# Optimization experiments

Hardware: AMD Instinct MI355X
Metric: run time of the kernel (lower is better)

The kernel has to match this reference:

```python
import jax, jax.numpy as jnp
import numpy as np

H = 512   # n_hidden
V = 32000 # n_words
T1 = 128  # encoder length
T2 = 64   # decoder length
B = 32    # batch


def _gru_cell(x, h, W_ih, W_hh, b_ih, b_hh):
    # PyTorch GRUCell math. x: [B, in], h: [B, H]
    gi = x @ W_ih.T + b_ih            # [B, 3H]
    gh = h @ W_hh.T + b_hh            # [B, 3H]
    i_r, i_z, i_n = jnp.split(gi, 3, axis=-1)
    h_r, h_z, h_n = jnp.split(gh, 3, axis=-1)
    r = jax.nn.sigmoid(i_r + h_r)
    z = jax.nn.sigmoid(i_z + h_z)
    n = jnp.tanh(i_n + r * h_n)
    return (1.0 - z) * n + z * h


def setup_inputs() -> dict:
    key = jax.random.key(0)
    ks = jax.random.split(key, 18)
    s = 0.05
    f32 = jnp.float32
    return {
        "decoder_inputs": jax.random.randint(ks[0], (T2, B), 0, V),
        "state": jax.random.normal(ks[1], (2, B, H), f32),
        "encoder_outputs": jax.random.normal(ks[2], (T1, B, H), f32),
        "emb": jax.random.normal(ks[3], (V, H), f32) * s,
        "wa_W": jax.random.normal(ks[4], (H, 2 * H), f32) * s,
        "wa_b": jax.random.normal(ks[5], (H,), f32) * s,
        "va_W": jax.random.normal(ks[6], (1, H), f32) * s,
        "W_ih0": jax.random.normal(ks[7], (3 * H, 2 * H), f32) * s,
        "W_hh0": jax.random.normal(ks[8], (3 * H, H), f32) * s,
        "b_ih0": jax.random.normal(ks[9], (3 * H,), f32) * s,
        "b_hh0": jax.random.normal(ks[10], (3 * H,), f32) * s,
        "W_ih1": jax.random.normal(ks[11], (3 * H, H), f32) * s,
        "W_hh1": jax.random.normal(ks[12], (3 * H, H), f32) * s,
        "b_ih1": jax.random.normal(ks[13], (3 * H,), f32) * s,
        "b_hh1": jax.random.normal(ks[14], (3 * H,), f32) * s,
        "out_W": jax.random.normal(ks[15], (V, H), f32) * s,
        "out_b": jax.random.normal(ks[16], (V,), f32) * s,
    }


def reference(decoder_inputs, state, encoder_outputs, emb, wa_W, wa_b, va_W,
              W_ih0, W_hh0, b_ih0, b_hh0, W_ih1, W_hh1, b_ih1, b_hh1,
              out_W, out_b):
    x = emb[decoder_inputs]                               # [T2, B, H]
    # wa(concat([xt_rep, enc])) == xt @ Wx.T + enc @ We.T + b  (split the weight)
    Wx = wa_W[:, :H]                                      # [H, H]
    We = wa_W[:, H:]                                      # [H, H]
    enc_proj = jnp.einsum('tbh,oh->tbo', encoder_outputs, We) + wa_b  # [T1,B,H]
    va = va_W[0]                                          # [H]

    def step(h, xt):  # h: [2,B,H], xt: [B,H]
        u = jnp.tanh(xt @ Wx.T + enc_proj)                # [T1, B, H]
        e = jnp.einsum('tbh,h->tb', u, va)                # [T1, B]
        score = jax.nn.softmax(e, axis=0)                 # softmax over T1
        att_v = jnp.einsum('tbh,tb->bh', encoder_outputs, score)  # [B, H]
        gin = jnp.concatenate([xt, att_v], axis=-1)       # [B, 2H]
        h0 = _gru_cell(gin, h[0], W_ih0, W_hh0, b_ih0, b_hh0)
        h1 = _gru_cell(h0, h[1], W_ih1, W_hh1, b_ih1, b_hh1)
        return jnp.stack([h0, h1]), (h1, score)

    h_final, (ys, scores) = jax.lax.scan(step, state, x)  # ys: [T2, B, H]
    y = jnp.einsum('tbh,vh->tbv', ys, out_W) + out_b      # [T2, B, V]
    last_score = scores[-1][:, :, None]                   # [T1, B, 1] (torch returns last-step score)
    return y, h_final, last_score
```

## Files before the change

kernel.cpp:

```cpp
#include <hip/hip_runtime.h>
#include <hip/hip_bf16.h>
#include <hip/hip_cooperative_groups.h>
#include <stdint.h>

namespace cg = cooperative_groups;

#define HH   512
#define VV   32000
#define T1N  128
#define T2N  64
#define BB   32

typedef __attribute__((ext_vector_type(8))) short short8;
typedef __attribute__((ext_vector_type(4))) float f32x4;

__device__ __forceinline__ ushort f2b(float f) {
  unsigned u = __float_as_uint(f);
  unsigned r = (u + 0x7fffu + ((u >> 16) & 1u)) >> 16;
  return (ushort)r;
}
__device__ __forceinline__ float blo(unsigned u){ return __uint_as_float(u << 16); }
__device__ __forceinline__ float bhi(unsigned u){ return __uint_as_float(u & 0xffff0000u); }

__device__ __forceinline__ float fast_tanh(float x) {
  float ax = fabsf(x);
  float e  = __expf(-2.f * ax);
  float t  = (1.f - e) / (1.f + e);
  return x < 0.f ? -t : t;
}
__device__ __forceinline__ float fsig(float x) { return 1.f / (1.f + __expf(-x)); }

__global__ __launch_bounds__(256) void k_cvt(const float* __restrict__ s, ushort* __restrict__ d, int n) {
  int i = (blockIdx.x * 256 + threadIdx.x) * 4;
  if (i < n) {
    float4 v = *(const float4*)(s + i);
    ushort4 o = { f2b(v.x), f2b(v.y), f2b(v.z), f2b(v.w) };
    *(ushort4*)(d + i) = o;
  }
}

__global__ __launch_bounds__(256) void k_cvt_wa(const float* __restrict__ wa,
                                                ushort* __restrict__ Wx, ushort* __restrict__ We) {
  int i = (blockIdx.x * 256 + threadIdx.x) * 4;
  int half = (i >= HH * HH);
  int j = i & (HH * HH - 1);
  int o = j >> 9, c = j & 511;
  const float* s = wa + (size_t)o * 1024 + c + (half ? 512 : 0);
  float4 v = *(const float4*)s;
  ushort4 ov = { f2b(v.x), f2b(v.y), f2b(v.z), f2b(v.w) };
  *(ushort4*)((half ? We : Wx) + j) = ov;
}

__global__ __launch_bounds__(256) void k_embed(const int* __restrict__ toks, const float* __restrict__ emb,
                                               ushort* __restrict__ ginB) {
  int i = (blockIdx.x * 256 + threadIdx.x) * 4;
  int row = i >> 9, c = i & 511;
  int tok = toks[row];
  float4 v = *(const float4*)(emb + (size_t)tok * HH + c);
  ushort4 ov = { f2b(v.x), f2b(v.y), f2b(v.z), f2b(v.w) };
  *(ushort4*)(ginB + (size_t)row * 1024 + c) = ov;
}

__global__ __launch_bounds__(256) void k_gemm(const ushort* __restrict__ A, int lda,
                                              const ushort* __restrict__ B,
                                              const float* __restrict__ bias,
                                              float* __restrict__ C, int ldc, int K) {
  __shared__ ushort sA[128 * 32];
  __shared__ ushort sB[128 * 32];
  const int tid  = threadIdx.x;
  const int bm   = blockIdx.y * 128;
  const int bn   = blockIdx.x * 128;
  const int lane = tid & 63;
  const int wave = tid >> 6;
  const int wm   = (wave >> 1) * 64;
  const int wn   = (wave & 1) * 64;
  const int m16  = lane & 15;
  const int quad = lane >> 4;

  f32x4 acc[4][4] = {};

  for (int k0 = 0; k0 < K; k0 += 32) {
#pragma unroll
    for (int q = 0; q < 2; ++q) {
      int idx = q * 256 + tid;
      int row = idx >> 2;
      int kc  = (idx & 3) << 3;
      uint4 va = *(const uint4*)(A + (size_t)(bm + row) * lda + k0 + kc);
      *(uint4*)(&sA[idx * 8]) = va;
      uint4 vb = *(const uint4*)(B + (size_t)(bn + row) * K + k0 + kc);
      *(uint4*)(&sB[idx * 8]) = vb;
    }
    __syncthreads();
    short8 a[4], b[4];
#pragma unroll
    for (int i = 0; i < 4; ++i)
      a[i] = *(const short8*)(&sA[(wm + i * 16 + m16) * 32 + quad * 8]);
#pragma unroll
    for (int j = 0; j < 4; ++j)
      b[j] = *(const short8*)(&sB[(wn + j * 16 + m16) * 32 + quad * 8]);
#pragma unroll
    for (int i = 0; i < 4; ++i)
#pragma unroll
      for (int j = 0; j < 4; ++j)
        acc[i][j] = __builtin_amdgcn_mfma_f32_16x16x32_bf16(a[i], b[j], acc[i][j], 0, 0, 0);
    __syncthreads();
  }
#pragma unroll
  for (int i = 0; i < 4; ++i) {
    int gm = bm + wm + i * 16 + quad * 4;
#pragma unroll
    for (int j = 0; j < 4; ++j) {
      int gn = bn + wn + j * 16 + m16;
      float bv = bias ? bias[gn] : 0.f;
#pragma unroll
      for (int r = 0; r < 4; ++r)
        C[(size_t)(gm + r) * ldc + gn] = acc[i][j][r] + bv;
    }
  }
}

__global__ __launch_bounds__(256) void k_gemm_b16(const ushort* __restrict__ A, int lda,
                                                  const ushort* __restrict__ B,
                                                  const float* __restrict__ bias,
                                                  ushort* __restrict__ C, int ldc, int K) {
  __shared__ ushort sA[128 * 32];
  __shared__ ushort sB[128 * 32];
  const int tid  = threadIdx.x;
  const int bm   = blockIdx.y * 128;
  const int bn   = blockIdx.x * 128;
  const int lane = tid & 63;
  const int wave = tid >> 6;
  const int wm   = (wave >> 1) * 64;
  const int wn   = (wave & 1) * 64;
  const int m16  = lane & 15;
  const int quad = lane >> 4;

  f32x4 acc[4][4] = {};

  for (int k0 = 0; k0 < K; k0 += 32) {
#pragma unroll
    for (int q = 0; q < 2; ++q) {
      int idx = q * 256 + tid;
      int row = idx >> 2;
      int kc  = (idx & 3) << 3;
      uint4 va = *(const uint4*)(A + (size_t)(bm + row) * lda + k0 + kc);
      *(uint4*)(&sA[idx * 8]) = va;
      uint4 vb = *(const uint4*)(B + (size_t)(bn + row) * K + k0 + kc);
      *(uint4*)(&sB[idx * 8]) = vb;
    }
    __syncthreads();
    short8 a[4], b[4];
#pragma unroll
    for (int i = 0; i < 4; ++i)
      a[i] = *(const short8*)(&sA[(wm + i * 16 + m16) * 32 + quad * 8]);
#pragma unroll
    for (int j = 0; j < 4; ++j)
      b[j] = *(const short8*)(&sB[(wn + j * 16 + m16) * 32 + quad * 8]);
#pragma unroll
    for (int i = 0; i < 4; ++i)
#pragma unroll
      for (int j = 0; j < 4; ++j)
        acc[i][j] = __builtin_amdgcn_mfma_f32_16x16x32_bf16(a[i], b[j], acc[i][j], 0, 0, 0);
    __syncthreads();
  }
#pragma unroll
  for (int i = 0; i < 4; ++i) {
    int gm = bm + wm + i * 16 + quad * 4;
#pragma unroll
    for (int j = 0; j < 4; ++j) {
      int gn = bn + wn + j * 16 + m16;
      float bv = bias ? bias[gn] : 0.f;
#pragma unroll
      for (int r = 0; r < 4; ++r)
        C[(size_t)(gm + r) * ldc + gn] = f2b(acc[i][j][r] + bv);
    }
  }
}

__global__ __launch_bounds__(256) void k_scores(const float* __restrict__ xproj,
                                                const float* __restrict__ encp,
                                                const float* __restrict__ vaW,
                                                float* __restrict__ e) {
  int t2g = blockIdx.x >> 5;
  int b   = blockIdx.x & 31;
  __shared__ float sx[4][512];
  int tid = threadIdx.x;
  for (int i = tid; i < 4 * 512; i += 256) {
    int tt = i >> 9, h = i & 511;
    sx[tt][h] = xproj[((size_t)(t2g * 4 + tt) * BB + b) * HH + h];
  }
  __syncthreads();
  int lane = tid & 63, w = tid >> 6;
  int h8 = lane * 8;
  float va[8];
#pragma unroll
  for (int j = 0; j < 8; ++j) va[j] = vaW[h8 + j];
  for (int t1 = w; t1 < T1N; t1 += 4) {
    const float* ep = encp + ((size_t)t1 * BB + b) * HH + h8;
    float ev[8];
    *(float4*)&ev[0] = *(const float4*)ep;
    *(float4*)&ev[4] = *(const float4*)(ep + 4);
    float s0 = 0, s1 = 0, s2 = 0, s3 = 0;
#pragma unroll
    for (int j = 0; j < 8; ++j) {
      float epj = ev[j], vj = va[j];
      s0 += fast_tanh(sx[0][h8 + j] + epj) * vj;
      s1 += fast_tanh(sx[1][h8 + j] + epj) * vj;
      s2 += fast_tanh(sx[2][h8 + j] + epj) * vj;
      s3 += fast_tanh(sx[3][h8 + j] + epj) * vj;
    }
#pragma unroll
    for (int off = 32; off; off >>= 1) {
      s0 += __shfl_down(s0, off);
      s1 += __shfl_down(s1, off);
      s2 += __shfl_down(s2, off);
      s3 += __shfl_down(s3, off);
    }
    if (lane == 0) {
      size_t base = ((size_t)(t2g * 4) * BB + b) * T1N + t1;
      e[base]                 = s0;
      e[base + 1 * BB * T1N]  = s1;
      e[base + 2 * BB * T1N]  = s2;
      e[base + 3 * BB * T1N]  = s3;
    }
  }
}

__global__ __launch_bounds__(128) void k_softmax(const float* __restrict__ e, float* __restrict__ score,
                                                 float* __restrict__ out_last) {
  int row = blockIdx.x;
  int tid = threadIdx.x;
  float v = e[(size_t)row * T1N + tid];
  __shared__ float red[128];
  red[tid] = v; __syncthreads();
  for (int s = 64; s; s >>= 1) { if (tid < s) red[tid] = fmaxf(red[tid], red[tid + s]); __syncthreads(); }
  float mx = red[0]; __syncthreads();
  float p = __expf(v - mx);
  red[tid] = p; __syncthreads();
  for (int s = 64; s; s >>= 1) { if (tid < s) red[tid] += red[tid + s]; __syncthreads(); }
  float sc = p / red[0];
  score[(size_t)row * T1N + tid] = sc;
  if ((row >> 5) == T2N - 1) out_last[tid * BB + (row & 31)] = sc;
}

__global__ __launch_bounds__(256) void k_attv(const float* __restrict__ enc, const float* __restrict__ score,
                                              ushort* __restrict__ ginB) {
  int t2g = blockIdx.x >> 5;
  int b   = blockIdx.x & 31;
  __shared__ float ssc[8][T1N];
  int tid = threadIdx.x;
  for (int i = tid; i < 8 * T1N; i += 256) {
    int j = i >> 7, t1 = i & 127;
    ssc[j][t1] = score[((size_t)(t2g * 8 + j) * BB + b) * T1N + t1];
  }
  __syncthreads();
  float a0[8] = {}, a1[8] = {};
  for (int t1 = 0; t1 < T1N; ++t1) {
    const float* er = enc + ((size_t)t1 * BB + b) * HH;
    float e0 = er[tid], e1 = er[tid + 256];
#pragma unroll
    for (int j = 0; j < 8; ++j) { a0[j] += e0 * ssc[j][t1]; a1[j] += e1 * ssc[j][t1]; }
  }
#pragma unroll
  for (int j = 0; j < 8; ++j) {
    size_t r = (size_t)(t2g * 8 + j) * BB + b;
    ginB[r * 1024 + 512 + tid]       = f2b(a0[j]);
    ginB[r * 1024 + 512 + tid + 256] = f2b(a1[j]);
  }
}

__device__ __forceinline__ void gru_pair(uint gr, uint gz, uint gn, uint hr, uint hz, uint hn,
                                         float hold0, float hold1, float& o0, float& o1) {
  float r0 = fsig(blo(gr) + blo(hr));
  float r1 = fsig(bhi(gr) + bhi(hr));
  float z0 = fsig(blo(gz) + blo(hz));
  float z1 = fsig(bhi(gz) + bhi(hz));
  float n0 = fast_tanh(blo(gn) + r0 * blo(hn));
  float n1 = fast_tanh(bhi(gn) + r1 * bhi(hn));
  o0 = (1.f - z0) * n0 + z0 * hold0;
  o1 = (1.f - z1) * n1 + z1 * hold1;
}

struct RecurP {
  const ushort* Whh0B; const ushort* Whh1B; const ushort* Wih1B;
  const float* bhh0; const float* bhh1; const float* bih1;
  const ushort* gi0B;
  const float* state;
  const ushort* stateB;
  ushort* gh0x;
  ushort* gh1b0; ushort* gh1b1;
  ushort* gi1x;
  float* h0b0; float* h0b1;
  float* h1b0; float* h1b1;
  ushort* h0B0; ushort* h0B1;
  float* h_out;
  ushort* ysB;
};

__global__ __launch_bounds__(256, 1) void k_recur(RecurP p) {
  cg::grid_group grid = cg::this_grid();
  __shared__ ushort sH[32 * 520];
  const int tid  = threadIdx.x;
  const int blk  = blockIdx.x;
  const int lane = tid & 63, wave = tid >> 6;
  const int bt = wave & 1, nt = wave >> 1;
  const int m16 = lane & 15, quad = lane >> 4;
  const int nrow = blk * 32 + nt * 16 + m16;
  const int k0 = tid * 2;
  const float* state1 = p.state + BB * HH;

  const float bv0 = p.bhh0[nrow];
  const float bv1 = p.bhh1[nrow];
  const float bvi = p.bih1[nrow];
  const int brow = bt * 16 + quad * 4;

#pragma unroll 1
  for (int t = 0; t < T2N; ++t) {
    const int par = t & 1;
    if (t == 0) {
      for (int i = tid; i < 16384; i += 256) {
        int b = i >> 9, k = i & 511;
        sH[b * 520 + k] = f2b(state1[i]);
      }
    } else {
      const ushort* gh1in = par ? p.gh1b0 : p.gh1b1;
      const float*  h1in  = (t <= 1) ? state1 : (par ? p.h1b1 : p.h1b0);
      float*        h1out = par ? p.h1b0 : p.h1b1;
      ushort*       ysprev = p.ysB + (size_t)(t - 1) * BB * HH;
#pragma unroll 4
      for (int b = 0; b < 32; ++b) {
        const ushort* gi = p.gi1x + b * 1536 + k0;
        const ushort* gh = gh1in + b * 1536 + k0;
        uint gir = *(const uint*)(gi);
        uint giz = *(const uint*)(gi + 512);
        uint gin = *(const uint*)(gi + 1024);
        uint hr  = *(const uint*)(gh);
        uint hz  = *(const uint*)(gh + 512);
        uint hn  = *(const uint*)(gh + 1024);
        float2 hold = *(const float2*)(h1in + b * 512 + k0);
        float o0, o1;
        gru_pair(gir, giz, gin, hr, hz, hn, hold.x, hold.y, o0, o1);
        uint hb = (uint)f2b(o0) | ((uint)f2b(o1) << 16);
        *(uint*)(&sH[b * 520 + k0]) = hb;
        if (blk == b) {
          *(float2*)(h1out + b * 512 + k0) = make_float2(o0, o1);
          *(uint*)(ysprev + b * 512 + k0) = hb;
        }
      }
    }
    __syncthreads();

    {
      const ushort* h0Bin = (t == 0) ? p.stateB : (par ? p.h0B0 : p.h0B1);
      ushort* gh1out = par ? p.gh1b1 : p.gh1b0;
      f32x4 acc0 = {0.f, 0.f, 0.f, 0.f}, acc1 = {0.f, 0.f, 0.f, 0.f};
      const ushort* Arow0  = h0Bin + (bt * 16 + m16) * 512 + quad * 8;
      const ushort* Brow0  = p.Whh0B + (size_t)nrow * 512 + quad * 8;
      const ushort* Brow1  = p.Whh1B + (size_t)nrow * 512 + quad * 8;
      const ushort* sArow1 = &sH[(bt * 16 + m16) * 520 + quad * 8];
#pragma unroll 4
      for (int kc = 0; kc < 16; ++kc) {
        short8 a0 = *(const short8*)(Arow0 + kc * 32);
        short8 b0 = *(const short8*)(Brow0 + kc * 32);
        acc0 = __builtin_amdgcn_mfma_f32_16x16x32_bf16(a0, b0, acc0, 0, 0, 0);
        short8 a1 = *(const short8*)(sArow1 + kc * 32);
        short8 b1 = *(const short8*)(Brow1 + kc * 32);
        acc1 = __builtin_amdgcn_mfma_f32_16x16x32_bf16(a1, b1, acc1, 0, 0, 0);
      }
#pragma unroll
      for (int r = 0; r < 4; ++r) {
        p.gh0x[(brow + r) * 1536 + nrow] = f2b(acc0[r] + bv0);
        gh1out[(brow + r) * 1536 + nrow] = f2b(acc1[r] + bv1);
      }
    }
    grid.sync();

    {
      const ushort* gi0t  = p.gi0B + (size_t)t * 32 * 1536;
      const float*  h0in  = (t == 0) ? p.state : (par ? p.h0b0 : p.h0b1);
      float*        h0out = par ? p.h0b1 : p.h0b0;
      ushort*       h0Bout = par ? p.h0B1 : p.h0B0;
#pragma unroll 4
      for (int b = 0; b < 32; ++b) {
        const ushort* gi = gi0t + b * 1536 + k0;
        const ushort* gh = p.gh0x + b * 1536 + k0;
        uint gir = *(const uint*)(gi);
        uint giz = *(const uint*)(gi + 512);
        uint gin = *(const uint*)(gi + 1024);
        uint hr  = *(const uint*)(gh);
        uint hz  = *(const uint*)(gh + 512);
        uint hn  = *(const uint*)(gh + 1024);
        float2 hold = *(const float2*)(h0in + b * 512 + k0);
        float o0, o1;
        gru_pair(gir, giz, gin, hr, hz, hn, hold.x, hold.y, o0, o1);
        uint hb = (uint)f2b(o0) | ((uint)f2b(o1) << 16);
        *(uint*)(&sH[b * 520 + k0]) = hb;
        if (blk == b) {
          *(float2*)(h0out + b * 512 + k0) = make_float2(o0, o1);
          *(uint*)(h0Bout + b * 512 + k0) = hb;
        }
      }
      __syncthreads();

      f32x4 acc = {0.f, 0.f, 0.f, 0.f};
      const ushort* Brow  = p.Wih1B + (size_t)nrow * 512 + quad * 8;
      const ushort* sArow = &sH[(bt * 16 + m16) * 520 + quad * 8];
#pragma unroll 4
      for (int kc = 0; kc < 16; ++kc) {
        short8 a = *(const short8*)(sArow + kc * 32);
        short8 b = *(const short8*)(Brow + kc * 32);
        acc = __builtin_amdgcn_mfma_f32_16x16x32_bf16(a, b, acc, 0, 0, 0);
      }
#pragma unroll
      for (int r = 0; r < 4; ++r)
        p.gi1x[(brow + r) * 1536 + nrow] = f2b(acc[r] + bvi);
    }
    grid.sync();
  }

  if (blk < 32) {
    const int b = blk;
    const ushort* gi = p.gi1x + b * 1536 + k0;
    const ushort* gh = p.gh1b1 + b * 1536 + k0;
    uint gir = *(const uint*)(gi);
    uint giz = *(const uint*)(gi + 512);
    uint gin = *(const uint*)(gi + 1024);
    uint hr  = *(const uint*)(gh);
    uint hz  = *(const uint*)(gh + 512);
    uint hn  = *(const uint*)(gh + 1024);
    float2 hold = *(const float2*)(p.h1b0 + b * 512 + k0);
    float o0, o1;
    gru_pair(gir, giz, gin, hr, hz, hn, hold.x, hold.y, o0, o1);
    *(uint*)(p.ysB + (size_t)63 * BB * HH + b * 512 + k0) = (uint)f2b(o0) | ((uint)f2b(o1) << 16);
    p.h_out[16384 + b * 512 + k0]     = o0;
    p.h_out[16384 + b * 512 + k0 + 1] = o1;
    float2 h0p = *(const float2*)(p.h0b1 + b * 512 + k0);
    *(float2*)(p.h_out + b * 512 + k0) = h0p;
  }
}

extern "C" void kernel_launch(void* const* d_in, const int* in_sizes, int n_in,
                              void* d_out, int out_size, void* d_ws, size_t ws_size,
                              hipStream_t stream) {
  const int*   toks  = (const int*)d_in[0];
  const float* state = (const float*)d_in[1];
  const float* enc   = (const float*)d_in[2];
  const float* emb   = (const float*)d_in[3];
  const float* wa_W  = (const float*)d_in[4];
  const float* wa_b  = (const float*)d_in[5];
  const float* va    = (const float*)d_in[6];
  const float* b_ih0 = (const float*)d_in[9];
  const float* b_hh0 = (const float*)d_in[10];
  const float* b_ih1 = (const float*)d_in[13];
  const float* b_hh1 = (const float*)d_in[14];
  const float* out_W = (const float*)d_in[15];
  const float* out_b = (const float*)d_in[16];
  const float* W_ih0 = (const float*)d_in[7];
  const float* W_hh0 = (const float*)d_in[8];
  const float* W_ih1 = (const float*)d_in[11];
  const float* W_hh1 = (const float*)d_in[12];

  float* y_out  = (float*)d_out;
  float* h_out  = y_out + (size_t)T2N * BB * VV;
  float* ls_out = h_out + 2 * BB * HH;

  char* ws = (char*)d_ws;
  size_t off = 0;
  auto alloc = [&](size_t bytes) -> void* {
    void* p = ws + off;
    off += (bytes + 255) & ~(size_t)255;
    return p;
  };
  ushort* encB   = (ushort*)alloc((size_t)T1N * BB * HH * 2);
  ushort* ginB   = (ushort*)alloc((size_t)T2N * BB * 2 * HH * 2);
  ushort* WeB    = (ushort*)alloc((size_t)HH * HH * 2);
  ushort* WxB    = (ushort*)alloc((size_t)HH * HH * 2);
  ushort* Wih0B  = (ushort*)alloc((size_t)3 * HH * 2 * HH * 2);
  ushort* Whh0B  = (ushort*)alloc((size_t)3 * HH * HH * 2);
  ushort* Wih1B  = (ushort*)alloc((size_t)3 * HH * HH * 2);
  ushort* Whh1B  = (ushort*)alloc((size_t)3 * HH * HH * 2);
  ushort* outWB  = (ushort*)alloc((size_t)VV * HH * 2);
  ushort* stateB = (ushort*)alloc((size_t)BB * HH * 2);
  float* encproj = (float*)alloc((size_t)T1N * BB * HH * 4);
  float* xproj   = (float*)alloc((size_t)T2N * BB * HH * 4);
  float* eM      = (float*)alloc((size_t)T2N * BB * T1N * 4);
  float* score   = (float*)alloc((size_t)T2N * BB * T1N * 4);
  ushort* gi0B   = (ushort*)alloc((size_t)T2N * BB * 3 * HH * 2);
  ushort* gh0x   = (ushort*)alloc((size_t)BB * 3 * HH * 2);
  ushort* gh1buf0 = (ushort*)alloc((size_t)BB * 3 * HH * 2);
  ushort* gh1buf1 = (ushort*)alloc((size_t)BB * 3 * HH * 2);
  ushort* gi1x   = (ushort*)alloc((size_t)BB * 3 * HH * 2);
  float* h0buf0  = (float*)alloc((size_t)BB * HH * 4);
  float* h0buf1  = (float*)alloc((size_t)BB * HH * 4);
  float* h1buf0  = (float*)alloc((size_t)BB * HH * 4);
  float* h1buf1  = (float*)alloc((size_t)BB * HH * 4);
  ushort* h0bufB0 = (ushort*)alloc((size_t)BB * HH * 2);
  ushort* h0bufB1 = (ushort*)alloc((size_t)BB * HH * 2);
  ushort* ysB    = (ushort*)alloc((size_t)T2N * BB * HH * 2);

  k_cvt<<<VV * HH / 1024, 256, 0, stream>>>(out_W, outWB, VV * HH);
  k_cvt<<<T1N * BB * HH / 1024, 256, 0, stream>>>(enc, encB, T1N * BB * HH);
  k_cvt<<<3 * HH * 2 * HH / 1024, 256, 0, stream>>>(W_ih0, Wih0B, 3 * HH * 2 * HH);
  k_cvt<<<3 * HH * HH / 1024, 256, 0, stream>>>(W_hh0, Whh0B, 3 * HH * HH);
  k_cvt<<<3 * HH * HH / 1024, 256, 0, stream>>>(W_ih1, Wih1B, 3 * HH * HH);
  k_cvt<<<3 * HH * HH / 1024, 256, 0, stream>>>(W_hh1, Whh1B, 3 * HH * HH);
  k_cvt<<<BB * HH / 1024, 256, 0, stream>>>(state, stateB, BB * HH);
  k_cvt_wa<<<2 * HH * HH / 1024, 256, 0, stream>>>(wa_W, WxB, WeB);
  k_embed<<<T2N * BB * HH / 1024, 256, 0, stream>>>(toks, emb, ginB);

  k_gemm<<<dim3(HH / 128, T1N * BB / 128), 256, 0, stream>>>(encB, HH, WeB, wa_b, encproj, HH, HH);
  k_gemm<<<dim3(HH / 128, T2N * BB / 128), 256, 0, stream>>>(ginB, 2 * HH, WxB, nullptr, xproj, HH, HH);

  k_scores<<<512, 256, 0, stream>>>(xproj, encproj, va, eM);
  k_softmax<<<T2N * BB, 128, 0, stream>>>(eM, score, ls_out);
  k_attv<<<256, 256, 0, stream>>>(enc, score, ginB);

  k_gemm_b16<<<dim3(3 * HH / 128, T2N * BB / 128), 256, 0, stream>>>(ginB, 2 * HH, Wih0B, b_ih0, gi0B, 3 * HH, 2 * HH);

  RecurP rp;
  rp.Whh0B = Whh0B; rp.Whh1B = Whh1B; rp.Wih1B = Wih1B;
  rp.bhh0 = b_hh0; rp.bhh1 = b_hh1; rp.bih1 = b_ih1;
  rp.gi0B = gi0B;
  rp.state = state; rp.stateB = stateB;
  rp.gh0x = gh0x;
  rp.gh1b0 = gh1buf0; rp.gh1b1 = gh1buf1;
  rp.gi1x = gi1x;
  rp.h0b0 = h0buf0; rp.h0b1 = h0buf1;
  rp.h1b0 = h1buf0; rp.h1b1 = h1buf1;
  rp.h0B0 = h0bufB0; rp.h0B1 = h0bufB1;
  rp.h_out = h_out; rp.ysB = ysB;
  void* kargs[] = { &rp };
  hipLaunchCooperativeKernel((const void*)k_recur, dim3(48), dim3(256), kargs, 0, stream);

  k_gemm<<<dim3(VV / 128, T2N * BB / 128), 256, 0, stream>>>(ysB, HH, outWB, out_b, y_out, VV, HH);
}
```

Baseline: 4.500 ms.

## Cache recurrent weight slices in LDS and replace grid.sync with atomic barrier

After: 3.798 ms. 1.18x faster.

```diff
diff --git a/kernel.cpp b/kernel.cpp
--- a/kernel.cpp
+++ b/kernel.cpp
@@ -1,9 +1,6 @@
 #include <hip/hip_runtime.h>
 #include <hip/hip_bf16.h>
-#include <hip/hip_cooperative_groups.h>
 #include <stdint.h>
-
-namespace cg = cooperative_groups;
 
 #define HH   512
 #define VV   32000
@@ -281,6 +278,24 @@
   o1 = (1.f - z1) * n1 + z1 * hold1;
 }
 
+__device__ __forceinline__ void gbar(unsigned* bar, unsigned nblk) {
+  __syncthreads();
+  if (threadIdx.x == 0) {
+    unsigned g = __hip_atomic_load(bar + 16, __ATOMIC_RELAXED, __HIP_MEMORY_SCOPE_AGENT);
+    unsigned old = __hip_atomic_fetch_add(bar, 1u, __ATOMIC_ACQ_REL, __HIP_MEMORY_SCOPE_AGENT);
+    if (old == nblk - 1u) {
+      __hip_atomic_store(bar, 0u, __ATOMIC_RELAXED, __HIP_MEMORY_SCOPE_AGENT);
+      __hip_atomic_store(bar + 16, g + 1u, __ATOMIC_RELEASE, __HIP_MEMORY_SCOPE_AGENT);
+    } else {
+      while (__hip_atomic_load(bar + 16, __ATOMIC_ACQUIRE, __HIP_MEMORY_SCOPE_AGENT) == g)
+        __builtin_amdgcn_s_sleep(2);
+    }
+  }
+  __syncthreads();
+}
+
+__global__ void k_bar_init(unsigned* bar) { bar[0] = 0u; bar[16] = 0u; }
+
 struct RecurP {
   const ushort* Whh0B; const ushort* Whh1B; const ushort* Wih1B;
   const float* bhh0; const float* bhh1; const float* bih1;
@@ -295,11 +310,14 @@
   ushort* h0B0; ushort* h0B1;
   float* h_out;
   ushort* ysB;
+  unsigned* bar;
 };
 
 __global__ __launch_bounds__(256, 1) void k_recur(RecurP p) {
-  cg::grid_group grid = cg::this_grid();
   __shared__ ushort sH[32 * 520];
+  __shared__ ushort sW0[32 * 520];
+  __shared__ ushort sW1[32 * 520];
+  __shared__ ushort sWi[32 * 520];
   const int tid  = threadIdx.x;
   const int blk  = blockIdx.x;
   const int lane = tid & 63, wave = tid >> 6;
@@ -307,12 +325,21 @@
   const int m16 = lane & 15, quad = lane >> 4;
   const int nrow = blk * 32 + nt * 16 + m16;
   const int k0 = tid * 2;
+  const unsigned nblk = gridDim.x;
   const float* state1 = p.state + BB * HH;
 
   const float bv0 = p.bhh0[nrow];
   const float bv1 = p.bhh1[nrow];
   const float bvi = p.bih1[nrow];
   const int brow = bt * 16 + quad * 4;
+
+  for (int i = tid * 4; i < 32 * 512; i += 256 * 4) {
+    int row = i >> 9, col = i & 511;
+    size_t g = (size_t)(blk * 32 + row) * 512 + col;
+    *(uint2*)(&sW0[row * 520 + col]) = *(const uint2*)(p.Whh0B + g);
+    *(uint2*)(&sW1[row * 520 + col]) = *(const uint2*)(p.Whh1B + g);
+    *(uint2*)(&sWi[row * 520 + col]) = *(const uint2*)(p.Wih1B + g);
+  }
 
 #pragma unroll 1
   for (int t = 0; t < T2N; ++t) {
@@ -355,8 +382,8 @@
       ushort* gh1out = par ? p.gh1b1 : p.gh1b0;
       f32x4 acc0 = {0.f, 0.f, 0.f, 0.f}, acc1 = {0.f, 0.f, 0.f, 0.f};
       const ushort* Arow0  = h0Bin + (bt * 16 + m16) * 512 + quad * 8;
-      const ushort* Brow0  = p.Whh0B + (size_t)nrow * 512 + quad * 8;
-      const ushort* Brow1  = p.Whh1B + (size_t)nrow * 512 + quad * 8;
+      const ushort* Brow0  = &sW0[(nt * 16 + m16) * 520 + quad * 8];
+      const ushort* Brow1  = &sW1[(nt * 16 + m16) * 520 + quad * 8];
       const ushort* sArow1 = &sH[(bt * 16 + m16) * 520 + quad * 8];
 #pragma unroll 4
       for (int kc = 0; kc < 16; ++kc) {
@@ -373,7 +400,7 @@
         gh1out[(brow + r) * 1536 + nrow] = f2b(acc1[r] + bv1);
       }
     }
-    grid.sync();
+    gbar(p.bar, nblk);
 
     {
       const ushort* gi0t  = p.gi0B + (size_t)t * 32 * 1536;
@@ -403,7 +430,7 @@
       __syncthreads();
 
       f32x4 acc = {0.f, 0.f, 0.f, 0.f};
-      const ushort* Brow  = p.Wih1B + (size_t)nrow * 512 + quad * 8;
+      const ushort* Brow  = &sWi[(nt * 16 + m16) * 520 + quad * 8];
       const ushort* sArow = &sH[(bt * 16 + m16) * 520 + quad * 8];
 #pragma unroll 4
       for (int kc = 0; kc < 16; ++kc) {
@@ -415,7 +442,7 @@
       for (int r = 0; r < 4; ++r)
         p.gi1x[(brow + r) * 1536 + nrow] = f2b(acc[r] + bvi);
     }
-    grid.sync();
+    gbar(p.bar, nblk);
   }
 
   if (blk < 32) {
@@ -497,7 +524,9 @@
   ushort* h0bufB0 = (ushort*)alloc((size_t)BB * HH * 2);
   ushort* h0bufB1 = (ushort*)alloc((size_t)BB * HH * 2);
   ushort* ysB    = (ushort*)alloc((size_t)T2N * BB * HH * 2);
-
+  unsigned* bar  = (unsigned*)alloc(256);
+
+  k_bar_init<<<1, 1, 0, stream>>>(bar);
   k_cvt<<<VV * HH / 1024, 256, 0, stream>>>(out_W, outWB, VV * HH);
   k_cvt<<<T1N * BB * HH / 1024, 256, 0, stream>>>(enc, encB, T1N * BB * HH);
   k_cvt<<<3 * HH * 2 * HH / 1024, 256, 0, stream>>>(W_ih0, Wih0B, 3 * HH * 2 * HH);
@@ -529,6 +558,7 @@
   rp.h1b0 = h1buf0; rp.h1b1 = h1buf1;
   rp.h0B0 = h0bufB0; rp.h0B1 = h0bufB1;
   rp.h_out = h_out; rp.ysB = ysB;
+  rp.bar = bar;
   void* kargs[] = { &rp };
   hipLaunchCooperativeKernel((const void*)k_recur, dim3(48), dim3(256), kargs, 0, stream);
 
```

## Run GRU recurrence on six workgroups within one XCC using custom atomic barrier

Applied to the files above, without the earlier changes.

Result: slower. 6.501 ms (+44.5%).

```diff
diff --git a/kernel.cpp b/kernel.cpp
--- a/kernel.cpp
+++ b/kernel.cpp
@@ -1,15 +1,13 @@
 #include <hip/hip_runtime.h>
 #include <hip/hip_bf16.h>
-#include <hip/hip_cooperative_groups.h>
 #include <stdint.h>
-
-namespace cg = cooperative_groups;
 
 #define HH   512
 #define VV   32000
 #define T1N  128
 #define T2N  64
 #define BB   32
+#define NW   6
 
 typedef __attribute__((ext_vector_type(8))) short short8;
 typedef __attribute__((ext_vector_type(4))) float f32x4;
@@ -281,6 +279,33 @@
   o1 = (1.f - z1) * n1 + z1 * hold1;
 }
 
+__device__ __forceinline__ unsigned armw(unsigned* p, unsigned v) {
+  return __hip_atomic_fetch_add(p, v, __ATOMIC_RELAXED, __HIP_MEMORY_SCOPE_AGENT);
+}
+
+#define SPIN_GE(addr, target)                                             \
+  {                                                                       \
+    unsigned long long _t0 = __builtin_amdgcn_s_memrealtime();            \
+    while (armw((addr), 0u) < (target)) {                                 \
+      __builtin_amdgcn_s_sleep(1);                                        \
+      if (__builtin_amdgcn_s_memrealtime() - _t0 > 5000000ull) break;     \
+    }                                                                     \
+  }
+
+__device__ __forceinline__ void wbar(unsigned* cnt, unsigned ep) {
+  __syncthreads();
+  if (threadIdx.x == 0) {
+    armw(cnt, 1u);
+    SPIN_GE(cnt, NW * ep);
+    asm volatile("s_waitcnt vmcnt(0)\n\tbuffer_inv sc0\n\ts_waitcnt vmcnt(0)" ::: "memory");
+  }
+  __syncthreads();
+}
+
+__global__ void k_bar_init(unsigned* bs) {
+  for (int i = threadIdx.x; i < 512; i += 256) bs[i] = 0u;
+}
+
 struct RecurP {
   const ushort* Whh0B; const ushort* Whh1B; const ushort* Wih1B;
   const float* bhh0; const float* bhh1; const float* bih1;
@@ -290,29 +315,46 @@
   ushort* gh0x;
   ushort* gh1b0; ushort* gh1b1;
   ushort* gi1x;
-  float* h0b0; float* h0b1;
-  float* h1b0; float* h1b1;
-  ushort* h0B0; ushort* h0B1;
+  float* h0f;
+  float* h1f;
   float* h_out;
   ushort* ysB;
+  unsigned* bar;
 };
 
 __global__ __launch_bounds__(256, 1) void k_recur(RecurP p) {
-  cg::grid_group grid = cg::this_grid();
-  __shared__ ushort sH[32 * 520];
+  __shared__ ushort sH1[32 * 520];
+  __shared__ ushort sH0[32 * 520];
   const int tid  = threadIdx.x;
-  const int blk  = blockIdx.x;
   const int lane = tid & 63, wave = tid >> 6;
-  const int bt = wave & 1, nt = wave >> 1;
+  const int bt = wave & 1;
+  const int nh = wave >> 1;
   const int m16 = lane & 15, quad = lane >> 4;
-  const int nrow = blk * 32 + nt * 16 + m16;
   const int k0 = tid * 2;
+  unsigned* bs = p.bar;
   const float* state1 = p.state + BB * HH;
 
-  const float bv0 = p.bhh0[nrow];
-  const float bv1 = p.bhh1[nrow];
-  const float bvi = p.bih1[nrow];
-  const int brow = bt * 16 + quad * 4;
+  unsigned xcc;
+  asm volatile("s_getreg_b32 %0, hwreg(HW_REG_XCC_ID)" : "=s"(xcc));
+  xcc &= 7u;
+  __shared__ int s_wid;
+  if (tid == 0) {
+    unsigned rank = armw(bs + xcc * 16, 1u);
+    armw(bs + 128, 1u);
+    SPIN_GE(bs + 128, gridDim.x);
+    int chosen = -1;
+    for (int i = 0; i < 8; ++i)
+      if (chosen < 0 && armw(bs + (unsigned)i * 16, 0u) >= (unsigned)NW) chosen = i;
+    s_wid = (chosen == (int)xcc && rank < (unsigned)NW) ? (int)rank : -1;
+  }
+  __syncthreads();
+  const int wid = s_wid;
+  if (wid < 0) return;
+
+  float* h0f = p.h0f + (size_t)wid * (BB * HH);
+  float* h1f = p.h1f + (size_t)wid * (BB * HH);
+  const int browA = bt * 16 + quad * 4;
+  unsigned* cnt = bs + 144;
 
 #pragma unroll 1
   for (int t = 0; t < T2N; ++t) {
@@ -320,13 +362,13 @@
     if (t == 0) {
       for (int i = tid; i < 16384; i += 256) {
         int b = i >> 9, k = i & 511;
-        sH[b * 520 + k] = f2b(state1[i]);
+        sH1[b * 520 + k] = f2b(state1[i]);
+        sH0[b * 520 + k] = p.stateB[i];
       }
     } else {
       const ushort* gh1in = par ? p.gh1b0 : p.gh1b1;
-      const float*  h1in  = (t <= 1) ? state1 : (par ? p.h1b1 : p.h1b0);
-      float*        h1out = par ? p.h1b0 : p.h1b1;
-      ushort*       ysprev = p.ysB + (size_t)(t - 1) * BB * HH;
+      const float*  h1hold = (t == 1) ? state1 : h1f;
+      ushort* ysprev = p.ysB + (size_t)(t - 1) * BB * HH;
 #pragma unroll 4
       for (int b = 0; b < 32; ++b) {
         const ushort* gi = p.gi1x + b * 1536 + k0;
@@ -337,49 +379,58 @@
         uint hr  = *(const uint*)(gh);
         uint hz  = *(const uint*)(gh + 512);
         uint hn  = *(const uint*)(gh + 1024);
-        float2 hold = *(const float2*)(h1in + b * 512 + k0);
+        float2 hold = *(const float2*)(h1hold + b * 512 + k0);
         float o0, o1;
         gru_pair(gir, giz, gin, hr, hz, hn, hold.x, hold.y, o0, o1);
         uint hb = (uint)f2b(o0) | ((uint)f2b(o1) << 16);
-        *(uint*)(&sH[b * 520 + k0]) = hb;
-        if (blk == b) {
-          *(float2*)(h1out + b * 512 + k0) = make_float2(o0, o1);
-          *(uint*)(ysprev + b * 512 + k0) = hb;
-        }
+        *(uint*)(&sH1[b * 520 + k0]) = hb;
+        *(float2*)(h1f + b * 512 + k0) = make_float2(o0, o1);
+        if ((b % NW) == wid) *(uint*)(ysprev + b * 512 + k0) = hb;
       }
     }
     __syncthreads();
 
     {
-      const ushort* h0Bin = (t == 0) ? p.stateB : (par ? p.h0B0 : p.h0B1);
       ushort* gh1out = par ? p.gh1b1 : p.gh1b0;
-      f32x4 acc0 = {0.f, 0.f, 0.f, 0.f}, acc1 = {0.f, 0.f, 0.f, 0.f};
-      const ushort* Arow0  = h0Bin + (bt * 16 + m16) * 512 + quad * 8;
-      const ushort* Brow0  = p.Whh0B + (size_t)nrow * 512 + quad * 8;
-      const ushort* Brow1  = p.Whh1B + (size_t)nrow * 512 + quad * 8;
-      const ushort* sArow1 = &sH[(bt * 16 + m16) * 520 + quad * 8];
-#pragma unroll 4
-      for (int kc = 0; kc < 16; ++kc) {
-        short8 a0 = *(const short8*)(Arow0 + kc * 32);
-        short8 b0 = *(const short8*)(Brow0 + kc * 32);
-        acc0 = __builtin_amdgcn_mfma_f32_16x16x32_bf16(a0, b0, acc0, 0, 0, 0);
-        short8 a1 = *(const short8*)(sArow1 + kc * 32);
-        short8 b1 = *(const short8*)(Brow1 + kc * 32);
-        acc1 = __builtin_amdgcn_mfma_f32_16x16x32_bf16(a1, b1, acc1, 0, 0, 0);
+      short8 ar[16];
+#pragma unroll
+      for (int kc = 0; kc < 16; ++kc)
+        ar[kc] = *(const short8*)(&sH0[(bt * 16 + m16) * 520 + kc * 32 + quad * 8]);
+#pragma unroll 2
+      for (int i8 = 0; i8 < 8; ++i8) {
+        int nr = wid * 256 + nh * 128 + i8 * 16 + m16;
+        const ushort* Br = p.Whh0B + (size_t)nr * 512 + quad * 8;
+        f32x4 acc = {0.f, 0.f, 0.f, 0.f};
+#pragma unroll
+        for (int kc = 0; kc < 16; ++kc)
+          acc = __builtin_amdgcn_mfma_f32_16x16x32_bf16(ar[kc], *(const short8*)(Br + kc * 32), acc, 0, 0, 0);
+        float bv = p.bhh0[nr];
+#pragma unroll
+        for (int r = 0; r < 4; ++r)
+          p.gh0x[(browA + r) * 1536 + nr] = f2b(acc[r] + bv);
       }
 #pragma unroll
-      for (int r = 0; r < 4; ++r) {
-        p.gh0x[(brow + r) * 1536 + nrow] = f2b(acc0[r] + bv0);
-        gh1out[(brow + r) * 1536 + nrow] = f2b(acc1[r] + bv1);
+      for (int kc = 0; kc < 16; ++kc)
+        ar[kc] = *(const short8*)(&sH1[(bt * 16 + m16) * 520 + kc * 32 + quad * 8]);
+#pragma unroll 2
+      for (int i8 = 0; i8 < 8; ++i8) {
+        int nr = wid * 256 + nh * 128 + i8 * 16 + m16;
+        const ushort* Br = p.Whh1B + (size_t)nr * 512 + quad * 8;
+        f32x4 acc = {0.f, 0.f, 0.f, 0.f};
+#pragma unroll
+        for (int kc = 0; kc < 16; ++kc)
+          acc = __builtin_amdgcn_mfma_f32_16x16x32_bf16(ar[kc], *(const short8*)(Br + kc * 32), acc, 0, 0, 0);
+        float bv = p.bhh1[nr];
+#pragma unroll
+        for (int r = 0; r < 4; ++r)
+          gh1out[(browA + r) * 1536 + nr] = f2b(acc[r] + bv);
       }
     }
-    grid.sync();
+    wbar(cnt, (unsigned)(2 * t + 1));
 
     {
-      const ushort* gi0t  = p.gi0B + (size_t)t * 32 * 1536;
-      const float*  h0in  = (t == 0) ? p.state : (par ? p.h0b0 : p.h0b1);
-      float*        h0out = par ? p.h0b1 : p.h0b0;
-      ushort*       h0Bout = par ? p.h0B1 : p.h0B0;
+      const ushort* gi0t = p.gi0B + (size_t)t * 32 * 1536;
+      const float* h0hold = (t == 0) ? p.state : h0f;
 #pragma unroll 4
       for (int b = 0; b < 32; ++b) {
         const ushort* gi = gi0t + b * 1536 + k0;
@@ -390,36 +441,37 @@
         uint hr  = *(const uint*)(gh);
         uint hz  = *(const uint*)(gh + 512);
         uint hn  = *(const uint*)(gh + 1024);
-        float2 hold = *(const float2*)(h0in + b * 512 + k0);
+        float2 hold = *(const float2*)(h0hold + b * 512 + k0);
         float o0, o1;
         gru_pair(gir, giz, gin, hr, hz, hn, hold.x, hold.y, o0, o1);
         uint hb = (uint)f2b(o0) | ((uint)f2b(o1) << 16);
-        *(uint*)(&sH[b * 520 + k0]) = hb;
-        if (blk == b) {
-          *(float2*)(h0out + b * 512 + k0) = make_float2(o0, o1);
-          *(uint*)(h0Bout + b * 512 + k0) = hb;
-        }
+        *(uint*)(&sH0[b * 520 + k0]) = hb;
+        *(float2*)(h0f + b * 512 + k0) = make_float2(o0, o1);
       }
       __syncthreads();
 
-      f32x4 acc = {0.f, 0.f, 0.f, 0.f};
-      const ushort* Brow  = p.Wih1B + (size_t)nrow * 512 + quad * 8;
-      const ushort* sArow = &sH[(bt * 16 + m16) * 520 + quad * 8];
-#pragma unroll 4
-      for (int kc = 0; kc < 16; ++kc) {
-        short8 a = *(const short8*)(sArow + kc * 32);
-        short8 b = *(const short8*)(Brow + kc * 32);
-        acc = __builtin_amdgcn_mfma_f32_16x16x32_bf16(a, b, acc, 0, 0, 0);
+      short8 ar[16];
+#pragma unroll
+      for (int kc = 0; kc < 16; ++kc)
+        ar[kc] = *(const short8*)(&sH0[(bt * 16 + m16) * 520 + kc * 32 + quad * 8]);
+#pragma unroll 2
+      for (int i8 = 0; i8 < 8; ++i8) {
+        int nr = wid * 256 + nh * 128 + i8 * 16 + m16;
+        const ushort* Br = p.Wih1B + (size_t)nr * 512 + quad * 8;
+        f32x4 acc = {0.f, 0.f, 0.f, 0.f};
+#pragma unroll
+        for (int kc = 0; kc < 16; ++kc)
+          acc = __builtin_amdgcn_mfma_f32_16x16x32_bf16(ar[kc], *(const short8*)(Br + kc * 32), acc, 0, 0, 0);
+        float bv = p.bih1[nr];
+#pragma unroll
+        for (int r = 0; r < 4; ++r)
+          p.gi1x[(browA + r) * 1536 + nr] = f2b(acc[r] + bv);
       }
-#pragma unroll
-      for (int r = 0; r < 4; ++r)
-        p.gi1x[(brow + r) * 1536 + nrow] = f2b(acc[r] + bvi);
-    }
-    grid.sync();
-  }
-
-  if (blk < 32) {
-    const int b = blk;
+    }
+    wbar(cnt, (unsigned)(2 * t + 2));
+  }
+
+  for (int b = wid; b < 32; b += NW) {
     const ushort* gi = p.gi1x + b * 1536 + k0;
     const ushort* gh = p.gh1b1 + b * 1536 + k0;
     uint gir = *(const uint*)(gi);
@@ -428,13 +480,13 @@
     uint hr  = *(const uint*)(gh);
     uint hz  = *(const uint*)(gh + 512);
     uint hn  = *(const uint*)(gh + 1024);
-    float2 hold = *(const float2*)(p.h1b0 + b * 512 + k0);
+    float2 hold = *(const float2*)(h1f + b * 512 + k0);
     float o0, o1;
     gru_pair(gir, giz, gin, hr, hz, hn, hold.x, hold.y, o0, o1);
     *(uint*)(p.ysB + (size_t)63 * BB * HH + b * 512 + k0) = (uint)f2b(o0) | ((uint)f2b(o1) << 16);
     p.h_out[16384 + b * 512 + k0]     = o0;
     p.h_out[16384 + b * 512 + k0 + 1] = o1;
-    float2 h0p = *(const float2*)(p.h0b1 + b * 512 + k0);
+    float2 h0p = *(const float2*)(h0f + b * 512 + k0);
     *(float2*)(p.h_out + b * 512 + k0) = h0p;
   }
 }
@@ -490,14 +542,12 @@
   ushort* gh1buf0 = (ushort*)alloc((size_t)BB * 3 * HH * 2);
   ushort* gh1buf1 = (ushort*)alloc((size_t)BB * 3 * HH * 2);
   ushort* gi1x   = (ushort*)alloc((size_t)BB * 3 * HH * 2);
-  float* h0buf0  = (float*)alloc((size_t)BB * HH * 4);
-  float* h0buf1  = (float*)alloc((size_t)BB * HH * 4);
-  float* h1buf0  = (float*)alloc((size_t)BB * HH * 4);
-  float* h1buf1  = (float*)alloc((size_t)BB * HH * 4);
-  ushort* h0bufB0 = (ushort*)alloc((size_t)BB * HH * 2);
-  ushort* h0bufB1 = (ushort*)alloc((size_t)BB * HH * 2);
+  float* h0fw    = (float*)alloc((size_t)NW * BB * HH * 4);
+  float* h1fw    = (float*)alloc((size_t)NW * BB * HH * 4);
   ushort* ysB    = (ushort*)alloc((size_t)T2N * BB * HH * 2);
-
+  unsigned* bar  = (unsigned*)alloc(2048);
+
+  k_bar_init<<<1, 256, 0, stream>>>(bar);
   k_cvt<<<VV * HH / 1024, 256, 0, stream>>>(out_W, outWB, VV * HH);
   k_cvt<<<T1N * BB * HH / 1024, 256, 0, stream>>>(enc, encB, T1N * BB * HH);
   k_cvt<<<3 * HH * 2 * HH / 1024, 256, 0, stream>>>(W_ih0, Wih0B, 3 * HH * 2 * HH);
@@ -525,10 +575,9 @@
   rp.gh0x = gh0x;
   rp.gh1b0 = gh1buf0; rp.gh1b1 = gh1buf1;
   rp.gi1x = gi1x;
-  rp.h0b0 = h0buf0; rp.h0b1 = h0buf1;
-  rp.h1b0 = h1buf0; rp.h1b1 = h1buf1;
-  rp.h0B0 = h0bufB0; rp.h0B1 = h0bufB1;
+  rp.h0f = h0fw; rp.h1f = h1fw;
   rp.h_out = h_out; rp.ysB = ysB;
+  rp.bar = bar;
   void* kargs[] = { &rp };
   hipLaunchCooperativeKernel((const void*)k_recur, dim3(48), dim3(256), kargs, 0, stream);
 
```
